# Kernel tuning notes

Hardware: AMD Instinct MI355X
Metric: run time of the kernel (lower is better)

## Reference

```python
import jax, jax.numpy as jnp
import numpy as np

B, T, E, NH, NLEV = 16, 2048, 1024, 16, 12
HD = E // NH


def _level_matrix(length):
    # Vectorized version of get_level_index_weak (base=2): levels[t, s] for s < t.
    tt, ss = np.meshgrid(np.arange(length), np.arange(length), indexing='ij')
    t = tt.copy(); s = ss.copy()
    lev = np.zeros((length, length), dtype=np.int32)
    active = tt > ss
    while active.any():
        l = np.floor(np.log2(np.maximum(t, 1))).astype(np.int64)
        v = (1 << l)
        done = active & (s < v)
        lev[done] = (l[done] + 1).astype(np.int32)
        cont = active & ~done
        t = np.where(cont, t - v, t)
        s = np.where(cont, s - v, s)
        active = cont
    return lev  # lev[t,t] = 0 (diagonal uses level 0)


def setup_inputs() -> dict:
    key = jax.random.key(0)
    ks = jax.random.split(key, 12)
    s = 0.02
    inp = {
        'x': jax.random.normal(ks[0], (B, T, E), jnp.float32),
        'Wq': jax.random.normal(ks[1], (E, E), jnp.float32) * s,
        'bq': jnp.zeros((E,), jnp.float32),
        'Wk': jax.random.normal(ks[2], (E, E), jnp.float32) * s,
        'bk': jnp.zeros((E,), jnp.float32),
        'Wv': jax.random.normal(ks[3], (E, E), jnp.float32) * s,
        'bv': jnp.zeros((E,), jnp.float32),
        'A_log': jax.random.normal(ks[4], (T, NH), jnp.float32),
        'A_bias': jnp.zeros((T, NH), jnp.float32),
        'L': jax.random.normal(ks[5], (T, NH, NLEV), jnp.float32),
        'L_bias': jnp.zeros((T, NH, NLEV), jnp.float32),
        'Wo': jax.random.normal(ks[6], (E, E), jnp.float32) * s,
        'bo': jnp.zeros((E,), jnp.float32),
        'levels': jnp.asarray(_level_matrix(T)),
    }
    return inp


def reference(x, Wq, bq, Wk, bk, Wv, bv, A_log, A_bias, L, L_bias, Wo, bo, levels):
    Bn, Tn, En = x.shape
    NHh = A_log.shape[1]
    HDd = En // NHh
    # q/k projections exist in the original forward but are never used by the
    # hierarchical attention; keep only v (q/k are dead code -> omitted).
    v = (x @ Wv.T + bv).reshape(Bn, Tn, NHh, HDd).transpose(0, 2, 1, 3)  # [B,H,T,D]

    # Decay factors: prod(A[s+1:t+1]) == exp(cumsum(logA)[t] - cumsum(logA)[s]).
    A = jax.nn.sigmoid(A_log + A_bias)            # [T, H]
    cs = jnp.cumsum(jnp.log(A), axis=0)           # [T, H]
    decay = jnp.exp(cs[:, None, :] - cs[None, :, :])  # [t, s, H]; diag == 1

    # Hierarchical level weights: G[t, s, h] = (L + L_bias)[t, h, levels[t, s]].
    Le = L + L_bias                               # [T, H, NLEV]
    G = Le[jnp.arange(Tn)[:, None], :, levels]    # [t, s, H]

    causal = jnp.tril(jnp.ones((Tn, Tn), dtype=bool))[:, :, None]
    Hm = jnp.where(causal, G * decay, jnp.zeros((), x.dtype))  # [t, s, H]

    # Original softmaxes the full row (upper triangle is 0, not -inf) -> keep that.
    attn = jax.nn.softmax(Hm, axis=1)             # over source dim s
    out = jnp.einsum('tsh,bhsd->bhtd', attn, v)   # [B,H,T,D]
    out = out.transpose(0, 2, 1, 3).reshape(Bn, Tn, En)
    return out @ Wo.T + bo
```

## Files before the change

kernel.cpp:

```cpp
#include <hip/hip_runtime.h>
#include <stdint.h>

static constexpr int Bn = 16, Tn = 2048, En = 1024, NHn = 16, HDn = 64, NLEVn = 12;

typedef __attribute__((ext_vector_type(8))) short short8;
typedef __attribute__((ext_vector_type(4))) float floatx4;

__device__ __forceinline__ unsigned short f2bf(float f) {
  unsigned int u = __float_as_uint(f);
  u += 0x7fffu + ((u >> 16) & 1u);
  return (unsigned short)(u >> 16);
}
__device__ __forceinline__ float bf2f(unsigned short s) {
  return __uint_as_float(((unsigned int)s) << 16);
}

__device__ __forceinline__ void async16(const unsigned short* g, unsigned short* l) {
  __builtin_amdgcn_global_load_lds(
      (const __attribute__((address_space(1))) unsigned int*)g,
      (__attribute__((address_space(3))) unsigned int*)l, 16, 0, 0);
}

static constexpr int NX4 = Bn * Tn * En / 4;
static constexpr int NW4 = En * En / 4;

__global__ void k_pre(const float* __restrict__ x, unsigned short* __restrict__ xb,
                      const float* __restrict__ Wv, unsigned short* __restrict__ Wvb,
                      const float* __restrict__ Wo, unsigned short* __restrict__ Wob,
                      const float* __restrict__ A_log, const float* __restrict__ A_bias,
                      float* __restrict__ csT) {
  int blk = blockIdx.x;
  int tid = threadIdx.x;
  if (blk < 16) {
    int h = blk;
    __shared__ float part[256];
    float loc[8];
    float run = 0.f;
#pragma unroll
    for (int j = 0; j < 8; j++) {
      int t = tid * 8 + j;
      float xx = A_log[t * NHn + h] + A_bias[t * NHn + h];
      float ls = -log1pf(__expf(-xx));
      run += ls;
      loc[j] = run;
    }
    part[tid] = run;
    __syncthreads();
    for (int d = 1; d < 256; d <<= 1) {
      float v = (tid >= d) ? part[tid - d] : 0.f;
      __syncthreads();
      part[tid] += v;
      __syncthreads();
    }
    float off = (tid > 0) ? part[tid - 1] : 0.f;
#pragma unroll
    for (int j = 0; j < 8; j++) csT[(size_t)h * Tn + tid * 8 + j] = loc[j] + off;
    return;
  }
  int i = (blk - 16) * 256 + tid;
  const float* src;
  unsigned short* dst;
  int base;
  if (i < NX4) { src = x; dst = xb; base = 0; }
  else if (i < NX4 + NW4) { src = Wv; dst = Wvb; base = NX4; }
  else if (i < NX4 + 2 * NW4) { src = Wo; dst = Wob; base = NX4 + NW4; }
  else return;
  int k = i - base;
  float4 v = ((const float4*)src)[k];
  ushort4 o;
  o.x = f2bf(v.x); o.y = f2bf(v.y); o.z = f2bf(v.z); o.w = f2bf(v.w);
  ((ushort4*)dst)[k] = o;
}

__global__ void k_wt(const float* __restrict__ L, const float* __restrict__ Lb,
                     const int* __restrict__ levels, const float* __restrict__ csT,
                     unsigned short* __restrict__ P, float* __restrict__ denom,
                     const unsigned short* __restrict__ vt, float* __restrict__ Stail) {
  int tid = threadIdx.x;
  if (blockIdx.x < Tn) {
    int t = blockIdx.x;
    __shared__ float Lrow[NHn * NLEVn];
    __shared__ float cst[NHn];
    __shared__ float dsum[NHn];
    if (tid < NHn * NLEVn) Lrow[tid] = L[t * NHn * NLEVn + tid] + Lb[t * NHn * NLEVn + tid];
    if (tid < NHn) { cst[tid] = csT[(size_t)tid * Tn + t]; dsum[tid] = 0.f; }
    __syncthreads();
    int Bt = ((t >> 8) + 1) << 8;
    float acc[NHn];
#pragma unroll
    for (int h = 0; h < NHn; h++) acc[h] = 0.f;
    for (int s = tid; s < Bt; s += 256) {
      int lev = levels[(size_t)t * Tn + s];
      bool causal = (s <= t);
#pragma unroll
      for (int h = 0; h < NHn; h++) {
        float w = 1.f;
        if (causal) {
          float csr = csT[(size_t)h * Tn + s];
          float dec = __expf(cst[h] - csr);
          w = __expf(Lrow[h * NLEVn + lev] * dec);
        }
        unsigned short pb = f2bf(w);
        acc[h] += bf2f(pb);
        P[((size_t)h * Tn + t) * Tn + s] = pb;
      }
    }
    int lane = tid & 63;
#pragma unroll
    for (int h = 0; h < NHn; h++) {
      float v = acc[h];
      for (int o = 32; o > 0; o >>= 1) v += __shfl_down(v, o, 64);
      if (lane == 0) atomicAdd(&dsum[h], v);
    }
    __syncthreads();
    if (tid < NHn) denom[(size_t)tid * Tn + t] = dsum[tid] + (float)(Tn - Bt);
  } else {
    int row = blockIdx.x - Tn;
    __shared__ float C[8];
    short8 v = *(const short8*)&vt[(size_t)row * Tn + tid * 8];
    float p = 0.f;
#pragma unroll
    for (int e = 0; e < 8; e++) p += bf2f((unsigned short)v[e]);
#pragma unroll
    for (int o = 16; o > 0; o >>= 1) p += __shfl_xor(p, o, 64);
    if ((tid & 31) == 0) C[tid >> 5] = p;
    __syncthreads();
    if (tid < 8) {
      float s = 0.f;
      for (int k = tid + 1; k < 8; k++) s += C[k];
      int h = row >> 10, col = row & 1023;
      Stail[(size_t)h * 8192 + tid * 1024 + col] = s;
    }
  }
}

__global__ __launch_bounds__(512)
void k_gemm_v(const unsigned short* __restrict__ A, const unsigned short* __restrict__ Bm,
              const float* __restrict__ bias, unsigned short* __restrict__ vt) {
  __shared__ unsigned short smem[24576];
  unsigned short* As = smem;
  unsigned short* Bs = smem + 16384;
  const int K = 1024;
  int tid = threadIdx.x;
  int wave = tid >> 6, lane = tid & 63;
  int wm = wave >> 1, wn = wave & 1;

  int flat = blockIdx.y * 8 + blockIdx.x;
  int xcd = flat & 7, slot = flat >> 3;
  int strip = xcd * 16 + (slot >> 3);
  int nt = slot & 7;
  int bm = strip * 256, bn = nt * 128;

  floatx4 zero4 = {0.f, 0.f, 0.f, 0.f};
  floatx4 acc[4][4];
#pragma unroll
  for (int i = 0; i < 4; i++)
#pragma unroll
    for (int j = 0; j < 4; j++) acc[i][j] = zero4;

  for (int k0 = 0; k0 < K; k0 += 64) {
    __syncthreads();
#pragma unroll
    for (int j = 0; j < 4; j++) {
      int f = j * 512 + tid;
      int r = f >> 3, c = f & 7;
      int cg = c ^ (r & 7);
      async16(&A[(size_t)(bm + r) * K + k0 + cg * 8], &As[f * 8]);
    }
#pragma unroll
    for (int j = 0; j < 2; j++) {
      int f = j * 512 + tid;
      int r = f >> 3, c = f & 7;
      int cg = c ^ (r & 7);
      async16(&Bm[(size_t)(bn + r) * K + k0 + cg * 8], &Bs[f * 8]);
    }
    __syncthreads();
#pragma unroll
    for (int kk = 0; kk < 2; kk++) {
      short8 af[4], bfr[4];
      int cgk = kk * 4 + (lane >> 4);
#pragma unroll
      for (int i = 0; i < 4; i++) {
        int m = wm * 64 + i * 16 + (lane & 15);
        af[i] = *(const short8*)&As[m * 64 + ((cgk ^ (m & 7)) * 8)];
        int n = wn * 64 + i * 16 + (lane & 15);
        bfr[i] = *(const short8*)&Bs[n * 64 + ((cgk ^ (n & 7)) * 8)];
      }
#pragma unroll
      for (int i = 0; i < 4; i++)
#pragma unroll
        for (int j = 0; j < 4; j++)
          acc[i][j] = __builtin_amdgcn_mfma_f32_16x16x32_bf16(af[i], bfr[j], acc[i][j], 0, 0, 0);
    }
  }

  int b = bm >> 11, t0 = bm & 2047;
  unsigned short* Ct = smem;
  const int S = 264;
#pragma unroll 1
  for (int pass = 0; pass < 2; pass++) {
    __syncthreads();
    if (wn == pass) {
#pragma unroll
      for (int i = 0; i < 4; i++) {
#pragma unroll
        for (int j = 0; j < 4; j++) {
          int colL = j * 16 + (lane & 15);
          float bia = bias[bn + pass * 64 + colL];
          int rowb = wm * 64 + i * 16 + (lane >> 4) * 4;
          ushort4 p;
          p.x = f2bf(acc[i][j][0] + bia);
          p.y = f2bf(acc[i][j][1] + bia);
          p.z = f2bf(acc[i][j][2] + bia);
          p.w = f2bf(acc[i][j][3] + bia);
          *(ushort4*)&Ct[colL * S + rowb] = p;
        }
      }
    }
    __syncthreads();
#pragma unroll
    for (int cc = 0; cc < 4; cc++) {
      int colL = wave * 8 + cc * 2 + (lane >> 5);
      int gc = bn + pass * 64 + colL;
      int h = gc >> 6, d = gc & 63;
      int tt = (lane & 31) * 8;
      short8 v = *(const short8*)&Ct[colL * S + tt];
      *(short8*)&vt[((size_t)((h * Bn + b) * HDn + d)) * Tn + t0 + tt] = v;
    }
  }
}


#define STAGE_A(kt, half, buf)                                                   \
  {                                                                              \
    _Pragma("unroll")                                                            \
    for (int j_ = 0; j_ < 2; j_++) {                                             \
      int f_ = j_ * 512 + tid;                                                   \
      int r_ = f_ >> 3, c_ = f_ & 7;                                             \
      int cg_ = c_ ^ (r_ & 7);                                                   \
      async16(&Ap[(size_t)(bm + (half) * 128 + r_) * K + (kt) * 64 + cg_ * 8],   \
              &smem[(buf) * 32768 + ((half) * 128 + r_) * 64 + c_ * 8]);         \
    }                                                                            \
  }

#define STAGE_B(kt, half, buf)                                                   \
  {                                                                              \
    _Pragma("unroll")                                                            \
    for (int j_ = 0; j_ < 2; j_++) {                                             \
      int f_ = j_ * 512 + tid;                                                   \
      int r_ = f_ >> 3, c_ = f_ & 7;                                             \
      int cg_ = c_ ^ (r_ & 7);                                                   \
      async16(&Bp[(size_t)(bn + (half) * 128 + r_) * K + (kt) * 64 + cg_ * 8],   \
              &smem[(buf) * 32768 + 16384 + ((half) * 128 + r_) * 64 + c_ * 8]); \
    }                                                                            \
  }

#define LOAD_A(buf, Mh)                                                          \
  {                                                                              \
    _Pragma("unroll")                                                            \
    for (int ii_ = 0; ii_ < 4; ii_++) {                                          \
      int m_ = (Mh) * 128 + wm * 64 + ii_ * 16 + (lane & 15);                    \
      _Pragma("unroll")                                                          \
      for (int kk_ = 0; kk_ < 2; kk_++) {                                        \
        int cgk_ = kk_ * 4 + (lane >> 4);                                        \
        aR[ii_][kk_] =                                                           \
            *(const short8*)&smem[(buf) * 32768 + m_ * 64 + ((cgk_ ^ (m_ & 7)) * 8)]; \
      }                                                                          \
    }                                                                            \
  }

#define LOAD_B(buf, Nh)                                                          \
  {                                                                              \
    _Pragma("unroll")                                                            \
    for (int jj_ = 0; jj_ < 2; jj_++) {                                          \
      int n_ = (Nh) * 128 + wn * 32 + jj_ * 16 + (lane & 15);                    \
      _Pragma("unroll")                                                          \
      for (int kk_ = 0; kk_ < 2; kk_++) {                                        \
        int cgk_ = kk_ * 4 + (lane >> 4);                                        \
        bR[jj_][kk_] = *(const short8*)&smem[(buf) * 32768 + 16384 + n_ * 64 +   \
                                             ((cgk_ ^ (n_ & 7)) * 8)];           \
      }                                                                          \
    }                                                                            \
  }

#define MFMA16(Mh, Nh)                                                           \
  {                                                                              \
    __builtin_amdgcn_s_setprio(1);                                               \
    _Pragma("unroll")                                                            \
    for (int kk_ = 0; kk_ < 2; kk_++)                                            \
      _Pragma("unroll")                                                          \
      for (int ii_ = 0; ii_ < 4; ii_++)                                          \
        _Pragma("unroll")                                                        \
        for (int jj_ = 0; jj_ < 2; jj_++)                                        \
          acc[(Mh) * 4 + ii_][(Nh) * 2 + jj_] = __builtin_amdgcn_mfma_f32_16x16x32_bf16( \
              aR[ii_][kk_], bR[jj_][kk_], acc[(Mh) * 4 + ii_][(Nh) * 2 + jj_], 0, 0, 0); \
    __builtin_amdgcn_s_setprio(0);                                               \
  }

#define WAIT6 asm volatile("s_waitcnt vmcnt(6)" ::: "memory")
#define BAR                                                                      \
  {                                                                              \
    asm volatile("" ::: "memory");                                               \
    __builtin_amdgcn_s_barrier();                                                \
    asm volatile("" ::: "memory");                                               \
  }

#define KTILE_BODY(buf, nbuf, tn)                                                \
  {                                                                              \
                                  \
    STAGE_A(tn, 0, nbuf);                                                        \
    WAIT6; BAR;                                                                  \
    LOAD_A(buf, 0);                                                              \
    LOAD_B(buf, 0);                                                              \
    MFMA16(0, 0);                                                                \
    BAR;                                                                         \
                               \
    STAGE_B(tn, 0, nbuf);                                                        \
    WAIT6; BAR;                                                                  \
    LOAD_B(buf, 1);                                                              \
    MFMA16(0, 1);                                                                \
    BAR;                                                                         \
                               \
    STAGE_B(tn, 1, nbuf);                                                        \
    WAIT6; BAR;                                                                  \
    LOAD_A(buf, 1);                                                              \
    MFMA16(1, 1);                                                                \
    BAR;                                                                         \
                            \
    STAGE_A(tn, 1, nbuf);                                                        \
    WAIT6; BAR;                                                                  \
    LOAD_B(buf, 0);                                                              \
    MFMA16(1, 0);                                                                \
    BAR;                                                                         \
  }

__global__ __launch_bounds__(512, 2)
void k_gemm_attn(const unsigned short* __restrict__ P, const unsigned short* __restrict__ vt,
                 const float* __restrict__ denom, const float* __restrict__ Stail,
                 unsigned short* __restrict__ outp) {
  __shared__ unsigned short smem[65536];
  const int K = Tn;
  int tid = threadIdx.x;
  int wave = tid >> 6, lane = tid & 63;
  int wm = wave >> 2, wn = wave & 3;

  int flat = blockIdx.y * 8 + blockIdx.x;
  int xcd = flat & 7, slot = flat >> 3;
  int h = xcd * 2 + (slot >> 5);
  int mtraw = (slot >> 2) & 7;
  int mt = (slot & 32) ? (7 - mtraw) : mtraw;
  int nt = slot & 3;
  int bm = mt * 256, bn = nt * 256;

  const unsigned short* Ap = P + (size_t)h * Tn * Tn;
  const unsigned short* Bp = vt + (size_t)h * (Bn * HDn) * Tn;

  floatx4 zero4 = {0.f, 0.f, 0.f, 0.f};
  floatx4 acc[8][4];
#pragma unroll
  for (int i = 0; i < 8; i++)
#pragma unroll
    for (int j = 0; j < 4; j++) acc[i][j] = zero4;

  short8 aR[4][2], bR[2][2];

  STAGE_A(0, 0, 0);
  STAGE_B(0, 0, 0);
  STAGE_B(0, 1, 0);
  STAGE_A(0, 1, 0);

  const int nkb = 4 * (mt + 1);
  for (int t = 0; t < nkb; t++) {
    int buf = t & 1, nbuf = buf ^ 1;
    int tn = (t < nkb - 1) ? t + 1 : nkb - 1;
    KTILE_BODY(buf, nbuf, tn);
  }
  asm volatile("s_waitcnt vmcnt(0)" ::: "memory");

  float tl[4];
#pragma unroll
  for (int j = 0; j < 4; j++) {
    int col = bn + (j >> 1) * 128 + wn * 32 + (j & 1) * 16 + (lane & 15);
    tl[j] = Stail[(size_t)h * 8192 + mt * 1024 + col];
  }

#pragma unroll
  for (int i = 0; i < 8; i++) {
    int rb = bm + (i >> 2) * 128 + wm * 64 + (i & 3) * 16 + (lane >> 4) * 4;
#pragma unroll
    for (int r = 0; r < 4; r++) {
      int row = rb + r;
      float sc = 1.f / denom[(size_t)h * Tn + row];
#pragma unroll
      for (int j = 0; j < 4; j++) {
        int col = bn + (j >> 1) * 128 + wn * 32 + (j & 1) * 16 + (lane & 15);
        int b = col >> 6, d = col & 63;
        outp[((size_t)(b * Tn + row)) * En + h * HDn + d] = f2bf((acc[i][j][r] + tl[j]) * sc);
      }
    }
  }
}

__global__ __launch_bounds__(512, 2)
void k_gemm_out(const unsigned short* __restrict__ A, const unsigned short* __restrict__ Bm,
                const float* __restrict__ bias, float* __restrict__ out) {
  __shared__ unsigned short smem[65536];
  const int K = 1024, N = 1024;
  int tid = threadIdx.x;
  int wave = tid >> 6, lane = tid & 63;
  int wm = wave >> 2, wn = wave & 3;

  int flat = blockIdx.y * 8 + blockIdx.x;
  int wg = (flat & 7) * 64 + (flat >> 3);
  int mt = wg >> 2, nt = wg & 3;
  int bm = mt * 256, bn = nt * 256;

  const unsigned short* Ap = A;
  const unsigned short* Bp = Bm;

  floatx4 zero4 = {0.f, 0.f, 0.f, 0.f};
  floatx4 acc[8][4];
#pragma unroll
  for (int i = 0; i < 8; i++)
#pragma unroll
    for (int j = 0; j < 4; j++) acc[i][j] = zero4;

  short8 aR[4][2], bR[2][2];

  STAGE_A(0, 0, 0);
  STAGE_B(0, 0, 0);
  STAGE_B(0, 1, 0);
  STAGE_A(0, 1, 0);

  const int nk = K / 64;
  for (int t = 0; t < nk; t++) {
    int buf = t & 1, nbuf = buf ^ 1;
    int tn = (t < nk - 1) ? t + 1 : nk - 1;
    KTILE_BODY(buf, nbuf, tn);
  }
  asm volatile("s_waitcnt vmcnt(0)" ::: "memory");

#pragma unroll
  for (int i = 0; i < 8; i++) {
    int rb = bm + (i >> 2) * 128 + wm * 64 + (i & 3) * 16 + (lane >> 4) * 4;
#pragma unroll
    for (int r = 0; r < 4; r++) {
      int row = rb + r;
#pragma unroll
      for (int j = 0; j < 4; j++) {
        int col = bn + (j >> 1) * 128 + wn * 32 + (j & 1) * 16 + (lane & 15);
        out[(size_t)row * N + col] = acc[i][j][r] + bias[col];
      }
    }
  }
}

extern "C" void kernel_launch(void* const* d_in, const int* in_sizes, int n_in,
                              void* d_out, int out_size, void* d_ws, size_t ws_size,
                              hipStream_t stream) {
  const float* x      = (const float*)d_in[0];
  const float* Wv     = (const float*)d_in[5];
  const float* bv     = (const float*)d_in[6];
  const float* A_log  = (const float*)d_in[7];
  const float* A_bias = (const float*)d_in[8];
  const float* L      = (const float*)d_in[9];
  const float* Lb     = (const float*)d_in[10];
  const float* Wo     = (const float*)d_in[11];
  const float* bo     = (const float*)d_in[12];
  const int* levels   = (const int*)d_in[13];
  float* out = (float*)d_out;

  char* ws = (char*)d_ws;
  float* csT           = (float*)(ws + 0);
  float* denom         = (float*)(ws + 131072);
  unsigned short* Wvb  = (unsigned short*)(ws + 262144);
  unsigned short* Wob  = (unsigned short*)(ws + 2359296);
  unsigned short* xb   = (unsigned short*)(ws + 4456448);
  unsigned short* Pw   = (unsigned short*)(ws + 4456448);
  unsigned short* vt   = (unsigned short*)(ws + 138674176);
  unsigned short* outp = (unsigned short*)(ws + 205783040);
  if (ws_size < 272891904ULL) return;

  float* Stail = out + (33554432 - 131072);

  int npre = 16 + (NX4 + 2 * NW4) / 256;
  k_pre<<<npre, 256, 0, stream>>>(x, xb, Wv, Wvb, Wo, Wob, A_log, A_bias, csT);

  k_gemm_v<<<dim3(8, 128), 512, 0, stream>>>(xb, Wvb, bv, vt);

  k_wt<<<Tn + NHn * 1024, 256, 0, stream>>>(L, Lb, levels, csT, Pw, denom, vt, Stail);

  k_gemm_attn<<<dim3(8, 64), 512, 0, stream>>>(Pw, vt, denom, Stail, outp);

  k_gemm_out<<<dim3(8, 64), 512, 0, stream>>>(outp, Wob, bo, out);
}
```

Before: 511.0 us.

## Fuse V-projection GEMM with attention-weight generation in one interleaved launch

Merges the V projection GEMM and the per-row attention weight/denominator kernel into a single launch. Blocks are interleaved two weight rows per GEMM tile, so the memory-bound P-matrix writes can overlap with the MFMA-bound GEMM on the same CUs. The weight path now uses 512 threads per row. The column-tail sums are split into their own kernel because they depend on the finished V output. xb is moved to the outp region so it no longer aliases P, which is now written concurrently with the GEMM reading xb.

```diff
diff --git a/kernel.cpp b/kernel.cpp
--- a/kernel.cpp
+++ b/kernel.cpp
@@ -72,16 +72,42 @@
   ((ushort4*)dst)[k] = o;
 }
 
-__global__ void k_wt(const float* __restrict__ L, const float* __restrict__ Lb,
-                     const int* __restrict__ levels, const float* __restrict__ csT,
-                     unsigned short* __restrict__ P, float* __restrict__ denom,
-                     const unsigned short* __restrict__ vt, float* __restrict__ Stail) {
+__global__ void k_tail(const unsigned short* __restrict__ vt, float* __restrict__ Stail) {
+  int row = blockIdx.x;
   int tid = threadIdx.x;
-  if (blockIdx.x < Tn) {
-    int t = blockIdx.x;
-    __shared__ float Lrow[NHn * NLEVn];
-    __shared__ float cst[NHn];
-    __shared__ float dsum[NHn];
+  __shared__ float C[8];
+  short8 v = *(const short8*)&vt[(size_t)row * Tn + tid * 8];
+  float p = 0.f;
+#pragma unroll
+  for (int e = 0; e < 8; e++) p += bf2f((unsigned short)v[e]);
+#pragma unroll
+  for (int o = 16; o > 0; o >>= 1) p += __shfl_xor(p, o, 64);
+  if ((tid & 31) == 0) C[tid >> 5] = p;
+  __syncthreads();
+  if (tid < 8) {
+    float s = 0.f;
+    for (int k = tid + 1; k < 8; k++) s += C[k];
+    int h = row >> 10, col = row & 1023;
+    Stail[(size_t)h * 8192 + tid * 1024 + col] = s;
+  }
+}
+
+__global__ __launch_bounds__(512)
+void k_gvw(const unsigned short* __restrict__ A, const unsigned short* __restrict__ Bm,
+           const float* __restrict__ bias, unsigned short* __restrict__ vt,
+           const float* __restrict__ L, const float* __restrict__ Lb,
+           const int* __restrict__ levels, const float* __restrict__ csT,
+           unsigned short* __restrict__ P, float* __restrict__ denom) {
+  __shared__ unsigned short smem[24576];
+  int blk = blockIdx.x;
+  int tid = threadIdx.x;
+
+  if (blk % 3 != 2) {
+    int t = (blk / 3) * 2 + (blk % 3);
+    float* sm = (float*)smem;
+    float* Lrow = sm;
+    float* cst  = sm + 192;
+    float* dsum = sm + 208;
     if (tid < NHn * NLEVn) Lrow[tid] = L[t * NHn * NLEVn + tid] + Lb[t * NHn * NLEVn + tid];
     if (tid < NHn) { cst[tid] = csT[(size_t)tid * Tn + t]; dsum[tid] = 0.f; }
     __syncthreads();
@@ -89,7 +115,7 @@
     float acc[NHn];
 #pragma unroll
     for (int h = 0; h < NHn; h++) acc[h] = 0.f;
-    for (int s = tid; s < Bt; s += 256) {
+    for (int s = tid; s < Bt; s += 512) {
       int lev = levels[(size_t)t * Tn + s];
       bool causal = (s <= t);
 #pragma unroll
@@ -114,38 +140,16 @@
     }
     __syncthreads();
     if (tid < NHn) denom[(size_t)tid * Tn + t] = dsum[tid] + (float)(Tn - Bt);
-  } else {
-    int row = blockIdx.x - Tn;
-    __shared__ float C[8];
-    short8 v = *(const short8*)&vt[(size_t)row * Tn + tid * 8];
-    float p = 0.f;
-#pragma unroll
-    for (int e = 0; e < 8; e++) p += bf2f((unsigned short)v[e]);
-#pragma unroll
-    for (int o = 16; o > 0; o >>= 1) p += __shfl_xor(p, o, 64);
-    if ((tid & 31) == 0) C[tid >> 5] = p;
-    __syncthreads();
-    if (tid < 8) {
-      float s = 0.f;
-      for (int k = tid + 1; k < 8; k++) s += C[k];
-      int h = row >> 10, col = row & 1023;
-      Stail[(size_t)h * 8192 + tid * 1024 + col] = s;
-    }
-  }
-}
-
-__global__ __launch_bounds__(512)
-void k_gemm_v(const unsigned short* __restrict__ A, const unsigned short* __restrict__ Bm,
-              const float* __restrict__ bias, unsigned short* __restrict__ vt) {
-  __shared__ unsigned short smem[24576];
+    return;
+  }
+
   unsigned short* As = smem;
   unsigned short* Bs = smem + 16384;
   const int K = 1024;
-  int tid = threadIdx.x;
   int wave = tid >> 6, lane = tid & 63;
   int wm = wave >> 1, wn = wave & 1;
 
-  int flat = blockIdx.y * 8 + blockIdx.x;
+  int flat = blk / 3;
   int xcd = flat & 7, slot = flat >> 3;
   int strip = xcd * 16 + (slot >> 3);
   int nt = slot & 7;
@@ -307,26 +311,22 @@
 
 #define KTILE_BODY(buf, nbuf, tn)                                                \
   {                                                                              \
-                                  \
     STAGE_A(tn, 0, nbuf);                                                        \
     WAIT6; BAR;                                                                  \
     LOAD_A(buf, 0);                                                              \
     LOAD_B(buf, 0);                                                              \
     MFMA16(0, 0);                                                                \
     BAR;                                                                         \
-                               \
     STAGE_B(tn, 0, nbuf);                                                        \
     WAIT6; BAR;                                                                  \
     LOAD_B(buf, 1);                                                              \
     MFMA16(0, 1);                                                                \
     BAR;                                                                         \
-                               \
     STAGE_B(tn, 1, nbuf);                                                        \
     WAIT6; BAR;                                                                  \
     LOAD_A(buf, 1);                                                              \
     MFMA16(1, 1);                                                                \
     BAR;                                                                         \
-                            \
     STAGE_A(tn, 1, nbuf);                                                        \
     WAIT6; BAR;                                                                  \
     LOAD_B(buf, 0);                                                              \
@@ -475,9 +475,9 @@
   float* denom         = (float*)(ws + 131072);
   unsigned short* Wvb  = (unsigned short*)(ws + 262144);
   unsigned short* Wob  = (unsigned short*)(ws + 2359296);
-  unsigned short* xb   = (unsigned short*)(ws + 4456448);
   unsigned short* Pw   = (unsigned short*)(ws + 4456448);
   unsigned short* vt   = (unsigned short*)(ws + 138674176);
+  unsigned short* xb   = (unsigned short*)(ws + 205783040);
   unsigned short* outp = (unsigned short*)(ws + 205783040);
   if (ws_size < 272891904ULL) return;
 
@@ -486,9 +486,9 @@
   int npre = 16 + (NX4 + 2 * NW4) / 256;
   k_pre<<<npre, 256, 0, stream>>>(x, xb, Wv, Wvb, Wo, Wob, A_log, A_bias, csT);
 
-  k_gemm_v<<<dim3(8, 128), 512, 0, stream>>>(xb, Wvb, bv, vt);
-
-  k_wt<<<Tn + NHn * 1024, 256, 0, stream>>>(L, Lb, levels, csT, Pw, denom, vt, Stail);
+  k_gvw<<<3072, 512, 0, stream>>>(xb, Wvb, bv, vt, L, Lb, levels, csT, Pw, denom);
+
+  k_tail<<<NHn * 1024, 256, 0, stream>>>(vt, Stail);
 
   k_gemm_attn<<<dim3(8, 64), 512, 0, stream>>>(Pw, vt, denom, Stail, outp);
 
```

New measurement: 555.0 us. 8.6% more time.
